# Kernel tuning notes

Hardware: AMD Instinct MI355X
Metric: run time of the kernel (lower is better)

Reference implementation:

```python
import jax, jax.numpy as jnp
import numpy as np
from jax import lax

SCORE_THRESH = 0.05
NMS_THRESH = 0.5
DET_PER_IMG = 100
K_PRE = 2048  # pre-NMS candidate cap (batched_nms is never run on N*C dense candidates)
BBOX_XFORM_CLIP = float(np.log(1000.0 / 16.0))
WX, WY, WW, WH = 10.0, 10.0, 5.0, 5.0


def _decode(reg, props):
    # reg: [N, C, 4] deltas, props: [N, 4] xyxy -> [N, C, 4] xyxy (torchvision BoxCoder.decode)
    w = props[:, 2] - props[:, 0]
    h = props[:, 3] - props[:, 1]
    cx = props[:, 0] + 0.5 * w
    cy = props[:, 1] + 0.5 * h
    dx = reg[..., 0] / WX
    dy = reg[..., 1] / WY
    dw = jnp.minimum(reg[..., 2] / WW, BBOX_XFORM_CLIP)
    dh = jnp.minimum(reg[..., 3] / WH, BBOX_XFORM_CLIP)
    pcx = dx * w[:, None] + cx[:, None]
    pcy = dy * h[:, None] + cy[:, None]
    pw = jnp.exp(dw) * w[:, None]
    ph = jnp.exp(dh) * h[:, None]
    return jnp.stack([pcx - 0.5 * pw, pcy - 0.5 * ph, pcx + 0.5 * pw, pcy + 0.5 * ph], axis=-1)


def _pairwise_iou(b):
    # b: [K, 4] -> [K, K]
    area = (b[:, 2] - b[:, 0]) * (b[:, 3] - b[:, 1])
    lt = jnp.maximum(b[:, None, :2], b[None, :, :2])
    rb = jnp.minimum(b[:, None, 2:], b[None, :, 2:])
    wh = jnp.clip(rb - lt, 0.0)
    inter = wh[..., 0] * wh[..., 1]
    return inter / (area[:, None] + area[None, :] - inter)


def _greedy_nms(iou, valid, thresh):
    # boxes assumed sorted by descending score; valid: [K] bool initial keep mask
    K = iou.shape[0]
    idx = jnp.arange(K)
    def body(i, keep):
        sup = (iou[i] > thresh) & (idx > i) & keep[i]
        return keep & (~sup)
    return lax.fori_loop(0, K, body, valid)


def _process_image(logits, reg, props, img_h, img_w):
    # logits: [N, C], reg: [N, 4C], props: [N, 4]
    N, C = logits.shape
    scores = jax.nn.softmax(logits, axis=-1)[:, 1:]          # [N, C-1] drop background
    boxes = _decode(reg.reshape(N, C, 4), props)[:, 1:]      # [N, C-1, 4]
    boxes = jnp.stack([
        jnp.clip(boxes[..., 0], 0.0, img_w),
        jnp.clip(boxes[..., 1], 0.0, img_h),
        jnp.clip(boxes[..., 2], 0.0, img_w),
        jnp.clip(boxes[..., 3], 0.0, img_h),
    ], axis=-1)
    labels = jnp.broadcast_to(jnp.arange(1, C), (N, C - 1))
    boxes = boxes.reshape(-1, 4)       # [M, 4], M = N*(C-1)
    scores = scores.reshape(-1)
    labels = labels.reshape(-1)
    wd = boxes[:, 2] - boxes[:, 0]
    ht = boxes[:, 3] - boxes[:, 1]
    valid = (scores > SCORE_THRESH) & (wd >= 1.0) & (ht >= 1.0)  # score thresh + remove_small_boxes
    masked = jnp.where(valid, scores, -1.0)
    top_s, top_i = lax.top_k(masked, K_PRE)
    tb = boxes[top_i]
    tl = labels[top_i]
    tvalid = top_s > SCORE_THRESH
    # batched_nms via per-class coordinate offsets
    off = tl.astype(tb.dtype) * (jnp.max(tb) + 1.0)
    keep = _greedy_nms(_pairwise_iou(tb + off[:, None]), tvalid, NMS_THRESH)
    ks = jnp.where(keep, top_s, -1.0)
    fs, fi = lax.top_k(ks, DET_PER_IMG)
    fvalid = fs > SCORE_THRESH
    out_boxes = jnp.where(fvalid[:, None], tb[fi], 0.0)
    out_scores = jnp.where(fvalid, fs, 0.0)
    out_labels = jnp.where(fvalid, tl[fi], -1)
    return out_boxes, out_scores, out_labels


def setup_inputs() -> dict:
    key = jax.random.key(0)
    k1, k2, k3 = jax.random.split(key, 3)
    B, N, C, H, W = 8, 4000, 91, 800, 800
    pts = jax.random.uniform(k1, (B, N, 2, 2), dtype=jnp.float32, minval=0.0, maxval=float(W))
    proposals = jnp.concatenate([pts.min(axis=2), pts.max(axis=2)], axis=-1)  # valid xyxy
    class_logits = jax.random.normal(k2, (B * N, C), dtype=jnp.float32)
    box_regression = 0.5 * jax.random.normal(k3, (B * N, 4 * C), dtype=jnp.float32)
    return {"class_logits": class_logits, "box_regression": box_regression,
            "proposals": proposals, "img_h": H, "img_w": W}


def reference(class_logits, box_regression, proposals, img_h, img_w):
    B, N, _ = proposals.shape
    C = class_logits.shape[-1]
    logits = class_logits.reshape(B, N, C)
    reg = box_regression.reshape(B, N, 4 * C)
    fn = lambda l, r, p: _process_image(l, r, p, float(img_h), float(img_w))
    boxes, scores, labels = jax.vmap(fn)(logits, reg, proposals)
    return boxes, scores, labels
```

## Files before the change

### kernel.cpp

```cpp
#include <hip/hip_runtime.h>
#include <stdint.h>

typedef unsigned int u32;
typedef unsigned long long u64;
typedef __attribute__((ext_vector_type(2))) unsigned long long u64x2;

#define BIMG 8
#define NPROP 4000
#define NCLS 91
#define CM1 90
#define MCAND (NPROP * CM1)
#define KPRE 2048
#define NBUCKET 4096
#define NREP 8
#define SELCAP 16384
#define DETS 100
#define WLCAP 2048
#define SCORE_T 0.05f
#define NMS_T 0.5f
#define BBOX_CLIP 4.135166556742356f

#define HISTREP_OFF ((size_t)0)
#define BCNTREP_OFF (HISTREP_OFF + (size_t)NREP * BIMG * NBUCKET * 4)
#define META_OFF    (BCNTREP_OFF + (size_t)NREP * BIMG * NBUCKET * 4)
#define ZERO_BYTES  (META_OFF + 4096)
#define START_OFF   (ZERO_BYTES)
#define HISTTOT_OFF (START_OFF + (size_t)BIMG * NBUCKET * 4)
#define STARTREP_OFF (HISTTOT_OFF + (size_t)BIMG * NBUCKET * 4)
#define SEL_OFF     (STARTREP_OFF + (size_t)NREP * BIMG * NBUCKET * 4)
#define TBOX_OFF    (SEL_OFF + (size_t)BIMG * SELCAP * 8)
#define TSB_OFF     (TBOX_OFF + (size_t)BIMG * KPRE * 16)
#define TSC_OFF     (TSB_OFF + (size_t)BIMG * KPRE * 16)
#define TLB_OFF     (TSC_OFF + (size_t)BIMG * KPRE * 4)
#define TVL_OFF     (TLB_OFF + (size_t)BIMG * KPRE * 4)
#define KEEP_OFF    (TVL_OFF + (size_t)BIMG * KPRE * 4)
#define WLIST_OFF   (KEEP_OFF + (size_t)BIMG * 32 * 8)
#define UNION_OFF   (WLIST_OFF + (size_t)BIMG * WLCAP * 4)
#define UNION_BYTES ((size_t)BIMG * MCAND * 4)
#define MASK_BYTES  ((size_t)BIMG * KPRE * 32 * 8)
#define WS_NEED     (UNION_OFF + UNION_BYTES)

__device__ __forceinline__ void decode_clip(const float4 rg, const float w, const float h,
                                            const float cx, const float cy,
                                            const float fw, const float fh, float bx[4]) {
    float dx = rg.x / 10.0f;
    float dy = rg.y / 10.0f;
    float dw = fminf(rg.z / 5.0f, BBOX_CLIP);
    float dh = fminf(rg.w / 5.0f, BBOX_CLIP);
    float pcx = dx * w + cx;
    float pcy = dy * h + cy;
    float pw  = expf(dw) * w;
    float phh = expf(dh) * h;
    bx[0] = fminf(fmaxf(pcx - 0.5f * pw,  0.0f), fw);
    bx[1] = fminf(fmaxf(pcy - 0.5f * phh, 0.0f), fh);
    bx[2] = fminf(fmaxf(pcx + 0.5f * pw,  0.0f), fw);
    bx[3] = fminf(fmaxf(pcy + 0.5f * phh, 0.0f), fh);
}

__global__ __launch_bounds__(256) void k1_score_hist(
    const float* __restrict__ logits, const float* __restrict__ reg,
    const float* __restrict__ props, const int* __restrict__ imh, const int* __restrict__ imw,
    u32* __restrict__ histrep, u32* __restrict__ cand_ord) {
    const int lane = threadIdx.x & 63;
    const int pid = blockIdx.x * 4 + (threadIdx.x >> 6);
    if (pid >= BIMG * NPROP) return;
    const int img = pid / NPROP;
    const float fw = (float)imw[0], fh = (float)imh[0];
    const float* lrow = logits + (size_t)pid * NCLS;
    float v0 = lrow[lane];
    float v1 = (lane < 27) ? lrow[lane + 64] : -3.0e38f;
    float mx = fmaxf(v0, v1);
#pragma unroll
    for (int o = 32; o > 0; o >>= 1) mx = fmaxf(mx, __shfl_xor(mx, o));
    float es = expf(v0 - mx) + ((lane < 27) ? expf(v1 - mx) : 0.0f);
#pragma unroll
    for (int o = 32; o > 0; o >>= 1) es += __shfl_xor(es, o);
    const float thr = mx + logf(es) - 2.9967323f;
    float4 p = reinterpret_cast<const float4*>(props)[pid];
    const float w = p.z - p.x, h = p.w - p.y;
    const float cx = p.x + 0.5f * w, cy = p.y + 0.5f * h;
    const float4* rrow = reinterpret_cast<const float4*>(reg) + (size_t)pid * NCLS;
    const int n = pid - img * NPROP;
    u32* co = cand_ord + (size_t)img * MCAND + (size_t)n * CM1;
#pragma unroll
    for (int batch = 0; batch < 2; ++batch) {
        int ci = lane + batch * 64;
        if (ci < CM1) {
            int c = ci + 1;
            float l = lrow[c];
            u32 o = 0u;
            if (l > thr) {
                float sc = expf(l - mx) / es;
                float4 rg = rrow[c];
                float bx[4];
                decode_clip(rg, w, h, cx, cy, fw, fh, bx);
                bool valid = (sc > SCORE_T) && (bx[2] - bx[0] >= 1.0f) && (bx[3] - bx[1] >= 1.0f);
                if (valid) {
                    o = __float_as_uint(sc) | 0x80000000u;
                    u32 t = (u32)img * MCAND + (u32)n * CM1 + (u32)ci;
                    int rep = (int)((t >> 8) & (NREP - 1));
                    atomicAdd(&histrep[((size_t)rep * BIMG + img) * NBUCKET + (o >> 20)], 1u);
                }
            }
            co[ci] = o;
        }
    }
}

__global__ __launch_bounds__(256) void k2_scan(
    const u32* __restrict__ histrep, u32* __restrict__ histtot,
    u32* __restrict__ start, u32* __restrict__ startrep, u32* __restrict__ meta,
    u32* __restrict__ wlist) {
    const int img = blockIdx.x;
    const int td = threadIdx.x;
    const int lane = td & 63, wv = td >> 6;
    u32 cnt[16]; u32 tsum = 0;
#pragma unroll
    for (int k = 0; k < 16; ++k) {
        const int bk = NBUCKET - 1 - (td * 16 + k);
        u32 c = 0;
#pragma unroll
        for (int r = 0; r < NREP; ++r)
            c += histrep[((size_t)r * BIMG + img) * NBUCKET + bk];
        cnt[k] = c; tsum += c;
    }
    u32 inc = tsum;
#pragma unroll
    for (int o = 1; o < 64; o <<= 1) { u32 t = __shfl_up(inc, o); if (lane >= o) inc += t; }
    __shared__ u32 wsum[4];
    __shared__ u32 TbkS, Vs;
    if (td == 0) TbkS = 0u;
    if (lane == 63) wsum[wv] = inc;
    __syncthreads();
    u32 wbase = 0;
    for (int i = 0; i < wv; ++i) wbase += wsum[i];
    if (td == 255) Vs = wbase + inc;
    const u32 excl0 = wbase + inc - tsum;
    u32 excl = excl0;
#pragma unroll
    for (int k = 0; k < 16; ++k) {
        const int bk = NBUCKET - 1 - (td * 16 + k);
        const u32 c = cnt[k];
        start[img * NBUCKET + bk] = excl;
        histtot[img * NBUCKET + bk] = c;
        u32 sub = excl;
#pragma unroll
        for (int r = 0; r < NREP; ++r) {
            startrep[((size_t)r * BIMG + img) * NBUCKET + bk] = sub;
            sub += histrep[((size_t)r * BIMG + img) * NBUCKET + bk];
        }
        if (c > 0 && excl < KPRE && excl + c >= KPRE) TbkS = (u32)bk;
        excl += c;
    }
    u32 qcnt = 0;
    {
        u32 e = excl0;
#pragma unroll
        for (int k = 0; k < 16; ++k) {
            if (cnt[k] >= 2 && e < KPRE) ++qcnt;
            e += cnt[k];
        }
    }
    u32 qinc = qcnt;
#pragma unroll
    for (int o = 1; o < 64; o <<= 1) { u32 t = __shfl_up(qinc, o); if (lane >= o) qinc += t; }
    __shared__ u32 qws[4];
    if (lane == 63) qws[wv] = qinc;
    __syncthreads();
    u32 qbase = 0;
    for (int i = 0; i < wv; ++i) qbase += qws[i];
    u32 qoff = qbase + qinc - qcnt;
    {
        u32 e = excl0;
#pragma unroll
        for (int k = 0; k < 16; ++k) {
            const int bk = NBUCKET - 1 - (td * 16 + k);
            if (cnt[k] >= 2 && e < KPRE && qoff < WLCAP) wlist[img * WLCAP + (qoff++)] = (u32)bk;
            e += cnt[k];
        }
    }
    if (td == 255) meta[img * 8 + 3] = qbase + qinc;
    __syncthreads();
    if (td == 0) {
        u32 V = Vs;
        meta[img * 8 + 0] = V;
        meta[img * 8 + 1] = TbkS;
        meta[img * 8 + 2] = (V < KPRE) ? (KPRE - V) : 0u;
    }
}

__global__ __launch_bounds__(256) void k3_compact(
    const u32* __restrict__ cand_ord, const u32* __restrict__ startrep,
    const u32* __restrict__ meta, u32* __restrict__ bcntrep, u64* __restrict__ sel) {
    const u32 t = blockIdx.x * 256 + threadIdx.x;
    const int rep = (int)(blockIdx.x & (NREP - 1));
    if (t >= (u32)(BIMG * MCAND)) return;
    const int img = t / MCAND;
    const u32 idx = t - (u32)img * MCAND;
    const u32 o = cand_ord[t];
    if (!o) return;
    const u32 bk = o >> 20;
    if (bk < meta[img * 8 + 1]) return;
    const size_t ri = ((size_t)rep * BIMG + img) * NBUCKET + bk;
    const u32 pos = startrep[ri] + atomicAdd(&bcntrep[ri], 1u);
    if (pos < SELCAP)
        sel[(size_t)img * SELCAP + pos] = ((u64)o << 32) | (u32)(~idx);
}

__global__ __launch_bounds__(64) void k3b_fill(
    const u32* __restrict__ cand_ord, const u32* __restrict__ meta, u64* __restrict__ sel) {
    const int img = blockIdx.x;
    const u32 need = meta[img * 8 + 2];
    if (need == 0) return;
    const u32 V = meta[img * 8 + 0];
    const int lane = threadIdx.x;
    const u32 ORDN1 = 0x407FFFFFu;
    u32 filled = 0;
    for (u32 b0 = 0; b0 < MCAND && filled < need; b0 += 64) {
        u32 idx = b0 + lane;
        bool inv = (idx < MCAND) && (cand_ord[(size_t)img * MCAND + idx] == 0u);
        u64 bal = __ballot(inv);
        u32 pre = (u32)__popcll(bal & ((1ull << lane) - 1ull));
        if (inv && (filled + pre) < need)
            sel[(size_t)img * SELCAP + V + filled + pre] = ((u64)ORDN1 << 32) | (u32)(~idx);
        filled += (u32)__popcll(bal);
    }
}

__global__ __launch_bounds__(256) void k4_sortseg(
    const u32* __restrict__ histtot, const u32* __restrict__ start,
    const u32* __restrict__ meta, const u32* __restrict__ wlist, u64* __restrict__ sel) {
    __shared__ u64 arr[4096];
    const int img = blockIdx.y;
    const int tid = threadIdx.x;
    const u32 wcount = meta[img * 8 + 3];
    for (u32 wi = blockIdx.x; wi < wcount; wi += gridDim.x) {
        const u32 bk = (wi < WLCAP) ? wlist[img * WLCAP + wi] : 0u;
        u32 cnt = histtot[img * NBUCKET + bk];
        u32 st = start[img * NBUCKET + bk];
        if (cnt < 2 || st >= KPRE) continue;
        if (st + cnt > SELCAP) cnt = SELCAP - st;
        if (cnt > 4096) cnt = 4096;
        int n = 1;
        while (n < (int)cnt) n <<= 1;
        u64* seg = sel + (size_t)img * SELCAP + st;
        for (int i = tid; i < n; i += 256) arr[i] = (i < (int)cnt) ? seg[i] : 0ull;
        __syncthreads();
        for (int k = 2; k <= n; k <<= 1)
            for (int j = k >> 1; j > 0; j >>= 1) {
                for (int i = tid; i < n; i += 256) {
                    int ixj = i ^ j;
                    if (ixj > i) {
                        u64 a = arr[i], b = arr[ixj];
                        bool swp = ((i & k) == 0) ? (a < b) : (a > b);
                        if (swp) { arr[i] = b; arr[ixj] = a; }
                    }
                }
                __syncthreads();
            }
        for (int i = tid; i < (int)cnt; i += 256) seg[i] = arr[i];
        __syncthreads();
    }
}

__global__ __launch_bounds__(256) void k5_gather(
    const u64* __restrict__ sel, const float* __restrict__ reg, const float* __restrict__ props,
    const int* __restrict__ imh, const int* __restrict__ imw,
    float* __restrict__ tbox, float* __restrict__ tsb, float* __restrict__ tsc,
    int* __restrict__ tlb, u32* __restrict__ tvl) {
    const int img = blockIdx.x;
    const int tid = threadIdx.x;
    const float fw = (float)imw[0], fh = (float)imh[0];
    float bx[8][4];
    int lab[8];
    float lm = -3.0e38f;
#pragma unroll
    for (int t = 0; t < 8; ++t) {
        int s = t * 256 + tid;
        u64 key = sel[(size_t)img * SELCAP + s];
        u32 o = (u32)(key >> 32);
        u32 idx = ~((u32)key);
        u32 b = (o & 0x80000000u) ? (o & 0x7FFFFFFFu) : ~o;
        float sc = __uint_as_float(b);
        u32 n = idx / CM1;
        int c = (int)(idx - n * CM1) + 1;
        int pid = img * NPROP + (int)n;
        float4 p = reinterpret_cast<const float4*>(props)[pid];
        float w = p.z - p.x, h = p.w - p.y;
        float cx = p.x + 0.5f * w, cy = p.y + 0.5f * h;
        float4 rg = reinterpret_cast<const float4*>(reg)[(size_t)pid * NCLS + c];
        decode_clip(rg, w, h, cx, cy, fw, fh, bx[t]);
        lab[t] = c;
        lm = fmaxf(lm, fmaxf(fmaxf(bx[t][0], bx[t][1]), fmaxf(bx[t][2], bx[t][3])));
        reinterpret_cast<float4*>(tbox)[(size_t)img * KPRE + s] =
            make_float4(bx[t][0], bx[t][1], bx[t][2], bx[t][3]);
        tsc[(size_t)img * KPRE + s] = sc;
        tlb[(size_t)img * KPRE + s] = c;
        tvl[(size_t)img * KPRE + s] = (sc > SCORE_T) ? 1u : 0u;
    }
#pragma unroll
    for (int o2 = 32; o2 > 0; o2 >>= 1) lm = fmaxf(lm, __shfl_xor(lm, o2));
    __shared__ float wm[4];
    if ((tid & 63) == 0) wm[tid >> 6] = lm;
    __syncthreads();
    float mplus = fmaxf(fmaxf(wm[0], wm[1]), fmaxf(wm[2], wm[3])) + 1.0f;
#pragma unroll
    for (int t = 0; t < 8; ++t) {
        int s = t * 256 + tid;
        float off = (float)lab[t] * mplus;
        reinterpret_cast<float4*>(tsb)[(size_t)img * KPRE + s] =
            make_float4(bx[t][0] + off, bx[t][1] + off, bx[t][2] + off, bx[t][3] + off);
    }
}

__global__ __launch_bounds__(64) void k6_mask(
    const float* __restrict__ tsb, u64* __restrict__ mask) {
    if (blockIdx.x < blockIdx.y) return;
    const int img = blockIdx.z;
    const int j0 = blockIdx.x * 64;
    const int i0 = blockIdx.y * 64;
    const int tid = threadIdx.x;
    __shared__ float4 cb[64];
    __shared__ float ca[64];
    float4 c = reinterpret_cast<const float4*>(tsb)[(size_t)img * KPRE + j0 + tid];
    cb[tid] = c;
    ca[tid] = (c.z - c.x) * (c.w - c.y);
    __syncthreads();
    const int i = i0 + tid;
    float4 r = reinterpret_cast<const float4*>(tsb)[(size_t)img * KPRE + i];
    float ra = (r.z - r.x) * (r.w - r.y);
    u64 bits = 0ull;
#pragma unroll 8
    for (int jj = 0; jj < 64; ++jj) {
        int j = j0 + jj;
        float4 cc = cb[jj];
        float wv = fmaxf(fminf(r.z, cc.z) - fmaxf(r.x, cc.x), 0.0f);
        float hv = fmaxf(fminf(r.w, cc.w) - fmaxf(r.y, cc.y), 0.0f);
        float inter = wv * hv;
        float iou = inter / ((ra + ca[jj]) - inter);
        if ((iou > NMS_T) && (j > i)) bits |= (1ull << jj);
    }
    mask[((size_t)img * KPRE + i) * 32 + (j0 >> 6)] = bits;
}

__device__ __forceinline__ u64 rdlane64(u64 v, int l) {
    u32 lo = (u32)__builtin_amdgcn_readlane((int)(u32)v, l);
    u32 hi = (u32)__builtin_amdgcn_readlane((int)(u32)(v >> 32), l);
    return ((u64)hi << 32) | lo;
}

__device__ __forceinline__ void g2l16(const void* g, void* l) {
    __builtin_amdgcn_global_load_lds(
        (const __attribute__((address_space(1))) void*)g,
        (__attribute__((address_space(3))) void*)l, 16, 0, 0);
}

__global__ __launch_bounds__(64) void k7_nms(
    const u64* __restrict__ mask, const u32* __restrict__ tvl, u64* __restrict__ keepw) {
    __shared__ u64 lbuf[2][2048];
    const int img = blockIdx.x;
    const int lane = threadIdx.x;
    const int lg = lane >> 4;
    const u64* mrow = mask + (size_t)img * KPRE * 32;

    u64 accx = 0ull, accy = 0ull, rp = 0ull;
    for (int w = 0; w < 32; ++w) {
        bool tv = tvl[(size_t)img * KPRE + w * 64 + lane] != 0u;
        u64 iw = ~__ballot(tv);
        if (w == 0) rp = iw;
        if ((lane & 15) == (w >> 1)) { if (w & 1) accy = iw; else accx = iw; }
    }

    {
        const char* gsrc = (const char*)mrow + (size_t)lane * 16;
#pragma unroll
        for (int t = 0; t < 16; ++t)
            g2l16(gsrc + (size_t)t * 1024, (char*)&lbuf[0][0] + (size_t)t * 1024);
    }
    u64 diag = mrow[(size_t)lane * 32];

    u32 tk = 0;
    int bcut = 31;

#pragma unroll 1
    for (int b = 0; b < 32; ++b) {
        const size_t base32 = (size_t)b * 2048;
        const u64* cbuf = &lbuf[b & 1][0];

        u64 diagn = 0ull;
        if (b + 1 < 32) {
            diagn = mrow[base32 + 2048 + (size_t)lane * 32 + (b + 1)];
            const char* gsrc = (const char*)(mrow + base32 + 2048) + (size_t)lane * 16;
            char* nb_l = (char*)&lbuf[(b + 1) & 1][0];
#pragma unroll
            for (int t = 0; t < 16; ++t)
                g2l16(gsrc + (size_t)t * 1024, nb_l + (size_t)t * 1024);
        }

        u64 A = rp;
#pragma unroll
        for (int u = 0; u < 64; ++u) {
            u64 row = rdlane64(diag, u);
            if (!((A >> u) & 1ull)) A |= row;
        }
        const u64 keptw = ~A;

        if (b + 1 < 32) asm volatile("s_waitcnt vmcnt(17)" ::: "memory");
        else            asm volatile("s_waitcnt vmcnt(0)" ::: "memory");

#define LDV(K) u64x2 v##K = *(const u64x2*)&cbuf[128 * (K) + 2 * lane];
#define PRV(K) { u32 nib = (u32)(keptw >> (4 * (K))) & 15u; \
                 u32 kb = (nib >> lg) & 1u; \
                 accx |= kb ? v##K.x : 0ull; accy |= kb ? v##K.y : 0ull; }
        LDV(0) LDV(1) LDV(2) LDV(3)
        LDV(4) LDV(5) LDV(6) LDV(7)     PRV(0) PRV(1) PRV(2) PRV(3)
        LDV(8) LDV(9) LDV(10) LDV(11)   PRV(4) PRV(5) PRV(6) PRV(7)
        LDV(12) LDV(13) LDV(14) LDV(15) PRV(8) PRV(9) PRV(10) PRV(11)
        PRV(12) PRV(13) PRV(14) PRV(15)
#undef LDV
#undef PRV

        tk += (u32)__popcll(keptw);
        if (tk >= (u32)DETS) { bcut = b; break; }

        const int nb2 = b + 1;
        if (nb2 < 32) {
            u64 asel = (nb2 & 1) ? accy : accx;
            const int sl = (nb2 >> 1) & 15;
            rp = rdlane64(asel, sl) | rdlane64(asel, sl + 16) |
                 rdlane64(asel, sl + 32) | rdlane64(asel, sl + 48);
        }
        diag = diagn;
    }

    asm volatile("s_waitcnt vmcnt(0)" ::: "memory");

    accx |= __shfl_xor(accx, 16); accx |= __shfl_xor(accx, 32);
    accy |= __shfl_xor(accy, 16); accy |= __shfl_xor(accy, 32);
    if (lane < 16) {
        keepw[img * 32 + 2 * lane]     = (2 * lane     <= bcut) ? ~accx : 0ull;
        keepw[img * 32 + 2 * lane + 1] = (2 * lane + 1 <= bcut) ? ~accy : 0ull;
    }
}

__global__ __launch_bounds__(64) void k8_select(
    const u64* __restrict__ keepw, const float* __restrict__ tsc,
    const float* __restrict__ tbox, const int* __restrict__ tlb,
    float* __restrict__ out) {
    const int img = blockIdx.x;
    const int lane = threadIdx.x;
    u64 kw = (lane < 32) ? keepw[img * 32 + lane] : 0ull;
    u32 cnt = (u32)__popcll(kw);
    u32 inc = cnt;
#pragma unroll
    for (int o = 1; o < 64; o <<= 1) { u32 t = __shfl_up(inc, o); if (lane >= o) inc += t; }
    const u32 excl = inc - cnt;
    const u32 total = (u32)__shfl(inc, 63);

    float* ob0 = out + (size_t)img * DETS * 4;
    float* os0 = out + (size_t)BIMG * DETS * 4 + (size_t)img * DETS;
    float* ol0 = out + (size_t)BIMG * DETS * 5 + (size_t)img * DETS;

#pragma unroll
    for (int t = 0; t < 2; ++t) {
        u32 r = (u32)lane + (u32)t * 64;
        if (r < DETS && r >= total) {
            reinterpret_cast<float4*>(ob0)[r] = make_float4(0.f, 0.f, 0.f, 0.f);
            os0[r] = 0.0f;
            ol0[r] = -1.0f;
        }
    }

    u64 w = kw;
    u32 r = excl;
    while (w != 0ull && r < DETS) {
        int p = __ffsll((unsigned long long)w) - 1;
        w &= (w - 1ull);
        u32 s = (u32)lane * 64u + (u32)p;
        reinterpret_cast<float4*>(ob0)[r] =
            reinterpret_cast<const float4*>(tbox)[(size_t)img * KPRE + s];
        os0[r] = tsc[(size_t)img * KPRE + s];
        ol0[r] = (float)tlb[(size_t)img * KPRE + s];
        ++r;
    }
}

extern "C" void kernel_launch(void* const* d_in, const int* in_sizes, int n_in,
                              void* d_out, int out_size, void* d_ws, size_t ws_size,
                              hipStream_t stream) {
    const float* logits = (const float*)d_in[0];
    const float* reg    = (const float*)d_in[1];
    const float* props  = (const float*)d_in[2];
    const int*   imh    = (const int*)d_in[3];
    const int*   imw    = (const int*)d_in[4];
    float* out = (float*)d_out;
    char* ws = (char*)d_ws;
    if (ws_size < WS_NEED) return;

    u32* histrep  = (u32*)(ws + HISTREP_OFF);
    u32* bcntrep  = (u32*)(ws + BCNTREP_OFF);
    u32* meta     = (u32*)(ws + META_OFF);
    u32* start    = (u32*)(ws + START_OFF);
    u32* histtot  = (u32*)(ws + HISTTOT_OFF);
    u32* startrep = (u32*)(ws + STARTREP_OFF);
    u64* sel  = (u64*)(ws + SEL_OFF);
    float* tbox = (float*)(ws + TBOX_OFF);
    float* tsb  = (float*)(ws + TSB_OFF);
    float* tsc  = (float*)(ws + TSC_OFF);
    int*   tlb  = (int*)(ws + TLB_OFF);
    u32*   tvl  = (u32*)(ws + TVL_OFF);
    u64*   keepw = (u64*)(ws + KEEP_OFF);
    u32*   wlist = (u32*)(ws + WLIST_OFF);
    u32*   cand_ord = (u32*)(ws + UNION_OFF);
    u64*   mask = (u64*)(ws + UNION_OFF);

    hipMemsetAsync(d_ws, 0, ZERO_BYTES, stream);

    k1_score_hist<<<BIMG * NPROP / 4, 256, 0, stream>>>(logits, reg, props, imh, imw,
                                                        histrep, cand_ord);
    k2_scan<<<BIMG, 256, 0, stream>>>(histrep, histtot, start, startrep, meta, wlist);
    k3_compact<<<(BIMG * MCAND) / 256, 256, 0, stream>>>(cand_ord, startrep, meta, bcntrep, sel);
    k3b_fill<<<BIMG, 64, 0, stream>>>(cand_ord, meta, sel);
    hipMemsetAsync(mask, 0, MASK_BYTES, stream);
    k4_sortseg<<<dim3(64, BIMG), 256, 0, stream>>>(histtot, start, meta, wlist, sel);
    k5_gather<<<BIMG, 256, 0, stream>>>(sel, reg, props, imh, imw, tbox, tsb, tsc, tlb, tvl);
    k6_mask<<<dim3(32, 32, BIMG), 64, 0, stream>>>(tsb, mask);
    k7_nms<<<BIMG, 64, 0, stream>>>(mask, tvl, keepw);
    k8_select<<<BIMG, 64, 0, stream>>>(keepw, tsc, tbox, tlb, out);
}
```

Baseline: 272.8 us.

## Fuse fill into compact, zero mask in k6, merge NMS with select

Three launches and a memset are removed. The invalid-candidate fill now runs in the first blocks of k3_compact. The lower-triangle mask tiles are zeroed inside k6_mask instead of by a separate memset of the whole mask. The final selection is appended to the NMS kernel, which passes keep words via shuffles instead of global memory. This cuts launch overhead and the memset traffic. The risk is that the fill loop in compact blocks 0-7 is serialized and may lengthen that kernel's tail.

```diff
diff --git a/kernel.cpp b/kernel.cpp
--- a/kernel.cpp
+++ b/kernel.cpp
@@ -37,7 +37,6 @@
 #define WLIST_OFF   (KEEP_OFF + (size_t)BIMG * 32 * 8)
 #define UNION_OFF   (WLIST_OFF + (size_t)BIMG * WLCAP * 4)
 #define UNION_BYTES ((size_t)BIMG * MCAND * 4)
-#define MASK_BYTES  ((size_t)BIMG * KPRE * 32 * 8)
 #define WS_NEED     (UNION_OFF + UNION_BYTES)
 
 __device__ __forceinline__ void decode_clip(const float4 rg, const float w, const float h,
@@ -156,10 +155,7 @@
     {
         u32 e = excl0;
 #pragma unroll
-        for (int k = 0; k < 16; ++k) {
-            if (cnt[k] >= 2 && e < KPRE) ++qcnt;
-            e += cnt[k];
-        }
+        for (int k = 0; k < 16; ++k) { if (cnt[k] >= 2 && e < KPRE) ++qcnt; e += cnt[k]; }
     }
     u32 qinc = qcnt;
 #pragma unroll
@@ -194,36 +190,39 @@
     const u32* __restrict__ meta, u32* __restrict__ bcntrep, u64* __restrict__ sel) {
     const u32 t = blockIdx.x * 256 + threadIdx.x;
     const int rep = (int)(blockIdx.x & (NREP - 1));
-    if (t >= (u32)(BIMG * MCAND)) return;
-    const int img = t / MCAND;
-    const u32 idx = t - (u32)img * MCAND;
-    const u32 o = cand_ord[t];
-    if (!o) return;
-    const u32 bk = o >> 20;
-    if (bk < meta[img * 8 + 1]) return;
-    const size_t ri = ((size_t)rep * BIMG + img) * NBUCKET + bk;
-    const u32 pos = startrep[ri] + atomicAdd(&bcntrep[ri], 1u);
-    if (pos < SELCAP)
-        sel[(size_t)img * SELCAP + pos] = ((u64)o << 32) | (u32)(~idx);
-}
-
-__global__ __launch_bounds__(64) void k3b_fill(
-    const u32* __restrict__ cand_ord, const u32* __restrict__ meta, u64* __restrict__ sel) {
-    const int img = blockIdx.x;
-    const u32 need = meta[img * 8 + 2];
-    if (need == 0) return;
-    const u32 V = meta[img * 8 + 0];
-    const int lane = threadIdx.x;
-    const u32 ORDN1 = 0x407FFFFFu;
-    u32 filled = 0;
-    for (u32 b0 = 0; b0 < MCAND && filled < need; b0 += 64) {
-        u32 idx = b0 + lane;
-        bool inv = (idx < MCAND) && (cand_ord[(size_t)img * MCAND + idx] == 0u);
-        u64 bal = __ballot(inv);
-        u32 pre = (u32)__popcll(bal & ((1ull << lane) - 1ull));
-        if (inv && (filled + pre) < need)
-            sel[(size_t)img * SELCAP + V + filled + pre] = ((u64)ORDN1 << 32) | (u32)(~idx);
-        filled += (u32)__popcll(bal);
+    if (t < (u32)(BIMG * MCAND)) {
+        const int img = t / MCAND;
+        const u32 idx = t - (u32)img * MCAND;
+        const u32 o = cand_ord[t];
+        if (o) {
+            const u32 bk = o >> 20;
+            if (bk >= meta[img * 8 + 1]) {
+                const size_t ri = ((size_t)rep * BIMG + img) * NBUCKET + bk;
+                const u32 pos = startrep[ri] + atomicAdd(&bcntrep[ri], 1u);
+                if (pos < SELCAP)
+                    sel[(size_t)img * SELCAP + pos] = ((u64)o << 32) | (u32)(~idx);
+            }
+        }
+    }
+    if (blockIdx.x < BIMG && threadIdx.x < 64) {
+        const int img = blockIdx.x;
+        const u32 need = meta[img * 8 + 2];
+        if (need != 0) {
+            const u32 V = meta[img * 8 + 0];
+            const int lane = threadIdx.x;
+            const u32 ORDN1 = 0x407FFFFFu;
+            u32 filled = 0;
+            for (u32 b0 = 0; b0 < MCAND && filled < need; b0 += 64) {
+                u32 idx = b0 + (u32)lane;
+                bool inv = (idx < MCAND) && (cand_ord[(size_t)img * MCAND + idx] == 0u);
+                u64 bal = __ballot(inv);
+                u32 pre = (u32)__popcll(bal & ((1ull << lane) - 1ull));
+                if (inv && (filled + pre) < need)
+                    sel[(size_t)img * SELCAP + V + filled + pre] =
+                        ((u64)ORDN1 << 32) | (u32)(~idx);
+                filled += (u32)__popcll(bal);
+            }
+        }
     }
 }
 
@@ -315,11 +314,15 @@
 
 __global__ __launch_bounds__(64) void k6_mask(
     const float* __restrict__ tsb, u64* __restrict__ mask) {
-    if (blockIdx.x < blockIdx.y) return;
     const int img = blockIdx.z;
+    const int tid = threadIdx.x;
+    if (blockIdx.x < blockIdx.y) {
+        const int i = blockIdx.y * 64 + tid;
+        mask[((size_t)img * KPRE + i) * 32 + blockIdx.x] = 0ull;
+        return;
+    }
     const int j0 = blockIdx.x * 64;
     const int i0 = blockIdx.y * 64;
-    const int tid = threadIdx.x;
     __shared__ float4 cb[64];
     __shared__ float ca[64];
     float4 c = reinterpret_cast<const float4*>(tsb)[(size_t)img * KPRE + j0 + tid];
@@ -355,9 +358,11 @@
         (__attribute__((address_space(3))) void*)l, 16, 0, 0);
 }
 
-__global__ __launch_bounds__(64) void k7_nms(
-    const u64* __restrict__ mask, const u32* __restrict__ tvl, u64* __restrict__ keepw) {
-    __shared__ u64 lbuf[2][2048];
+__global__ __launch_bounds__(64) void k7_nms_sel(
+    const u64* __restrict__ mask, const u32* __restrict__ tvl,
+    const float* __restrict__ tsc, const float* __restrict__ tbox,
+    const int* __restrict__ tlb, float* __restrict__ out) {
+    __shared__ u64 smem[4096];
     const int img = blockIdx.x;
     const int lane = threadIdx.x;
     const int lg = lane >> 4;
@@ -375,7 +380,7 @@
         const char* gsrc = (const char*)mrow + (size_t)lane * 16;
 #pragma unroll
         for (int t = 0; t < 16; ++t)
-            g2l16(gsrc + (size_t)t * 1024, (char*)&lbuf[0][0] + (size_t)t * 1024);
+            g2l16(gsrc + (size_t)t * 1024, (char*)smem + (size_t)t * 1024);
     }
     u64 diag = mrow[(size_t)lane * 32];
 
@@ -385,13 +390,13 @@
 #pragma unroll 1
     for (int b = 0; b < 32; ++b) {
         const size_t base32 = (size_t)b * 2048;
-        const u64* cbuf = &lbuf[b & 1][0];
+        const u64* cbuf = smem + (size_t)(b & 1) * 2048;
 
         u64 diagn = 0ull;
         if (b + 1 < 32) {
             diagn = mrow[base32 + 2048 + (size_t)lane * 32 + (b + 1)];
             const char* gsrc = (const char*)(mrow + base32 + 2048) + (size_t)lane * 16;
-            char* nb_l = (char*)&lbuf[(b + 1) & 1][0];
+            char* nb_l = (char*)(smem + (size_t)((b + 1) & 1) * 2048);
 #pragma unroll
             for (int t = 0; t < 16; ++t)
                 g2l16(gsrc + (size_t)t * 1024, nb_l + (size_t)t * 1024);
@@ -437,19 +442,12 @@
 
     accx |= __shfl_xor(accx, 16); accx |= __shfl_xor(accx, 32);
     accy |= __shfl_xor(accy, 16); accy |= __shfl_xor(accy, 32);
-    if (lane < 16) {
-        keepw[img * 32 + 2 * lane]     = (2 * lane     <= bcut) ? ~accx : 0ull;
-        keepw[img * 32 + 2 * lane + 1] = (2 * lane + 1 <= bcut) ? ~accy : 0ull;
-    }
-}
-
-__global__ __launch_bounds__(64) void k8_select(
-    const u64* __restrict__ keepw, const float* __restrict__ tsc,
-    const float* __restrict__ tbox, const int* __restrict__ tlb,
-    float* __restrict__ out) {
-    const int img = blockIdx.x;
-    const int lane = threadIdx.x;
-    u64 kw = (lane < 32) ? keepw[img * 32 + lane] : 0ull;
+
+    u64 mxv = __shfl(accx, (lane >> 1) & 15);
+    u64 myv = __shfl(accy, (lane >> 1) & 15);
+    u64 kw = (lane & 1) ? ~myv : ~mxv;
+    if (lane >= 32 || lane > bcut) kw = 0ull;
+
     u32 cnt = (u32)__popcll(kw);
     u32 inc = cnt;
 #pragma unroll
@@ -470,7 +468,6 @@
             ol0[r] = -1.0f;
         }
     }
-
     u64 w = kw;
     u32 r = excl;
     while (w != 0ull && r < DETS) {
@@ -509,7 +506,6 @@
     float* tsc  = (float*)(ws + TSC_OFF);
     int*   tlb  = (int*)(ws + TLB_OFF);
     u32*   tvl  = (u32*)(ws + TVL_OFF);
-    u64*   keepw = (u64*)(ws + KEEP_OFF);
     u32*   wlist = (u32*)(ws + WLIST_OFF);
     u32*   cand_ord = (u32*)(ws + UNION_OFF);
     u64*   mask = (u64*)(ws + UNION_OFF);
@@ -520,11 +516,8 @@
                                                         histrep, cand_ord);
     k2_scan<<<BIMG, 256, 0, stream>>>(histrep, histtot, start, startrep, meta, wlist);
     k3_compact<<<(BIMG * MCAND) / 256, 256, 0, stream>>>(cand_ord, startrep, meta, bcntrep, sel);
-    k3b_fill<<<BIMG, 64, 0, stream>>>(cand_ord, meta, sel);
-    hipMemsetAsync(mask, 0, MASK_BYTES, stream);
     k4_sortseg<<<dim3(64, BIMG), 256, 0, stream>>>(histtot, start, meta, wlist, sel);
     k5_gather<<<BIMG, 256, 0, stream>>>(sel, reg, props, imh, imw, tbox, tsb, tsc, tlb, tvl);
     k6_mask<<<dim3(32, 32, BIMG), 64, 0, stream>>>(tsb, mask);
-    k7_nms<<<BIMG, 64, 0, stream>>>(mask, tvl, keepw);
-    k8_select<<<BIMG, 64, 0, stream>>>(keepw, tsc, tbox, tlb, out);
-}
+    k7_nms_sel<<<BIMG, 64, 0, stream>>>(mask, tvl, tsc, tbox, tlb, out);
+}
```

Result: faster. 263.2 us (-3.5%).
